# Performance work log

Hardware: AMD Instinct MI355X
Metric: run time of the kernel (lower is better)

## Reference

```python
import jax, jax.numpy as jnp
import numpy as np

B, N, D_MODEL, ATT_DIM, H = 2, 2048, 1024, 1024, 8
HEAD_DIM = ATT_DIM // H


def setup_inputs() -> dict:
    key = jax.random.key(0)
    ks = jax.random.split(key, 10)
    s_in = 1.0 / np.sqrt(D_MODEL)
    s_att = 1.0 / np.sqrt(ATT_DIM)
    x = jax.random.normal(ks[0], (B, N, D_MODEL), dtype=jnp.float32)
    mask = jax.random.randint(ks[1], (B, 1, N, N), 0, 2) == 1
    Wq = jax.random.uniform(ks[2], (D_MODEL, ATT_DIM), jnp.float32, -s_in, s_in)
    bq = jnp.zeros((ATT_DIM,), jnp.float32)
    Wk = jax.random.uniform(ks[3], (D_MODEL, ATT_DIM), jnp.float32, -s_in, s_in)
    bk = jnp.zeros((ATT_DIM,), jnp.float32)
    Wv = jax.random.uniform(ks[4], (D_MODEL, ATT_DIM), jnp.float32, -s_in, s_in)
    bv = jnp.zeros((ATT_DIM,), jnp.float32)
    Wo = jax.random.uniform(ks[5], (ATT_DIM, D_MODEL), jnp.float32, -s_att, s_att)
    bo = jnp.zeros((D_MODEL,), jnp.float32)
    return {"x": x, "mask": mask, "Wq": Wq, "bq": bq, "Wk": Wk, "bk": bk,
            "Wv": Wv, "bv": bv, "Wo": Wo, "bo": bo}


def reference(x, mask, Wq, bq, Wk, bk, Wv, bv, Wo, bo):
    # x: [B, N, d_model]; dropout is identity (eval mode) for a deterministic baseline.
    b, n, d_model = x.shape
    scale = d_model ** (-0.5)  # NOTE: original scales by d_model, not head_dim

    def split_heads(t):  # [B, N, att] -> [B, H, N, head]
        return t.reshape(b, n, H, HEAD_DIM).transpose(0, 2, 1, 3)

    q = split_heads(x @ Wq + bq)
    k = split_heads(x @ Wk + bk)
    v = split_heads(x @ Wv + bv)
    score = jnp.einsum('bhqd,bhkd->bhqk', q, k) * scale
    score = jnp.where(mask, -jnp.inf, score)
    w = jax.nn.softmax(score, axis=-1)
    out = jnp.einsum('bhqk,bhkd->bhqd', w, v)            # [B, H, N, head]
    out = out.transpose(0, 2, 1, 3).reshape(b, n, ATT_DIM)
    return out @ Wo + bo
```

## Files before the change

### kernel.cpp

```cpp
#include <hip/hip_runtime.h>
#include <stdint.h>

typedef __bf16 bf16_t;
typedef bf16_t bf16x8 __attribute__((ext_vector_type(8)));
typedef bf16_t bf16x4 __attribute__((ext_vector_type(4)));
typedef float f32x4 __attribute__((ext_vector_type(4)));
typedef unsigned long long u64;

#define B_ 2
#define N_ 2048
#define DM 1024
#define H_ 8
#define HD 128

#define GLDS16(g, l) __builtin_amdgcn_global_load_lds(                      \
    (const __attribute__((address_space(1))) void*)(g),                     \
    (__attribute__((address_space(3))) void*)(l), 16, 0, 0)

#if __has_builtin(__builtin_amdgcn_exp2f)
#define EXP2F(x) __builtin_amdgcn_exp2f(x)
#else
#define EXP2F(x) exp2f(x)
#endif

__global__ void cvt_kernel(const float* __restrict__ in, bf16_t* __restrict__ out, int n8)
{
    int i = blockIdx.x * blockDim.x + threadIdx.x;
    if (i >= n8) return;
    const float4 a = *(const float4*)(in + (size_t)i * 8);
    const float4 b = *(const float4*)(in + (size_t)i * 8 + 4);
    bf16x8 o;
    o[0] = (bf16_t)a.x; o[1] = (bf16_t)a.y; o[2] = (bf16_t)a.z; o[3] = (bf16_t)a.w;
    o[4] = (bf16_t)b.x; o[5] = (bf16_t)b.y; o[6] = (bf16_t)b.z; o[7] = (bf16_t)b.w;
    *(bf16x8*)(out + (size_t)i * 8) = o;
}

__global__ void transpose_cvt(const float* __restrict__ W, bf16_t* __restrict__ Wt)
{
    __shared__ float t[32][33];
    const int tx = threadIdx.x & 31;
    const int ty = threadIdx.x >> 5;
    const int bx = blockIdx.x * 32;
    const int by = blockIdx.y * 32;
#pragma unroll
    for (int i = 0; i < 32; i += 8)
        t[ty + i][tx] = W[(size_t)(by + ty + i) * 1024 + bx + tx];
    __syncthreads();
#pragma unroll
    for (int i = 0; i < 32; i += 8)
        Wt[(size_t)(bx + ty + i) * 1024 + by + tx] = (bf16_t)t[tx][ty + i];
}

__global__ void mask_pack(const int* __restrict__ mask, u64* __restrict__ mb, int nwords)
{
    const int t = blockIdx.x * blockDim.x + threadIdx.x;
    const int w = t >> 6;
    if (w >= nwords) return;
    const int v = mask[(size_t)w * 64 + (t & 63)];
    const u64 bits = __ballot(v != 0);
    if ((t & 63) == 0) mb[w] = bits;
}

template<int MODE>
__global__ __launch_bounds__(256)
void gemm_bt(const bf16_t* __restrict__ A, const bf16_t* __restrict__ Bt,
             const float* __restrict__ b0, const float* __restrict__ b1,
             const float* __restrict__ b2,
             void* __restrict__ Cout, bf16_t* __restrict__ VtOut,
             const int M, const int N, const int K, const int ldc, const int gy)
{
    __shared__ bf16_t sA[2][128 * 32];
    __shared__ bf16_t sB[2][128 * 32];

    const int tid  = threadIdx.x;
    const int wv   = tid >> 6;
    const int lane = tid & 63;
    const int fr   = lane & 15;
    const int fk   = (lane >> 4) * 8;

    const int nwg = gridDim.x;
    const int swz = ((int)blockIdx.x & 7) * (nwg >> 3) + ((int)blockIdx.x >> 3);
    const int by  = swz % gy;
    const int bx  = swz / gy;

    const int row0 = bx * 128;
    const int col0 = by * 128;
    const int wr   = (wv >> 1) * 64;
    const int wc   = (wv & 1) * 64;

    const int srow = wv * 32 + (lane >> 2);
    const int scol = (lane & 3) * 8;

    const bf16_t* gA0 = A  + (size_t)(row0 + srow) * K + scol;
    const bf16_t* gA1 = gA0 + (size_t)16 * K;
    const bf16_t* gB0 = Bt + (size_t)(col0 + srow) * K + scol;
    const bf16_t* gB1 = gB0 + (size_t)16 * K;

    const int ldst0 = wv * 1024;
    const int ldst1 = wv * 1024 + 512;

    f32x4 acc[4][4] = {};
    const int NT = K >> 5;

    GLDS16(gA0, &sA[0][ldst0]);
    GLDS16(gA1, &sA[0][ldst1]);
    GLDS16(gB0, &sB[0][ldst0]);
    GLDS16(gB1, &sB[0][ldst1]);
    __syncthreads();

    for (int kt = 0; kt < NT; ++kt) {
        const int cur = kt & 1;
        if (kt + 1 < NT) {
            const size_t ko = (size_t)(kt + 1) * 32;
            GLDS16(gA0 + ko, &sA[cur ^ 1][ldst0]);
            GLDS16(gA1 + ko, &sA[cur ^ 1][ldst1]);
            GLDS16(gB0 + ko, &sB[cur ^ 1][ldst0]);
            GLDS16(gB1 + ko, &sB[cur ^ 1][ldst1]);
        }
        bf16x8 af[4], bfr[4];
#pragma unroll
        for (int i = 0; i < 4; ++i)
            af[i] = *(const bf16x8*)&sA[cur][(wr + i * 16 + fr) * 32 + fk];
#pragma unroll
        for (int i = 0; i < 4; ++i)
            bfr[i] = *(const bf16x8*)&sB[cur][(wc + i * 16 + fr) * 32 + fk];
#pragma unroll
        for (int i = 0; i < 4; ++i)
#pragma unroll
            for (int j = 0; j < 4; ++j)
                acc[i][j] = __builtin_amdgcn_mfma_f32_16x16x32_bf16(af[i], bfr[j], acc[i][j], 0, 0, 0);
        __syncthreads();
    }

#pragma unroll
    for (int i = 0; i < 4; ++i) {
#pragma unroll
        for (int j = 0; j < 4; ++j) {
            const int c = col0 + wc + j * 16 + fr;
            const int seg = c >> 10;
            const float bb = (seg == 0) ? b0[c] : (seg == 1 ? b1[c - 1024] : b2[c - 2048]);
#pragma unroll
            for (int r = 0; r < 4; ++r) {
                const int row = row0 + wr + i * 16 + (lane >> 4) * 4 + r;
                const float v = acc[i][j][r] + bb;
                if constexpr (MODE == 1) {
                    ((float*)Cout)[(size_t)row * ldc + c] = v;
                } else if constexpr (MODE == 0) {
                    ((bf16_t*)Cout)[(size_t)row * ldc + c] = (bf16_t)v;
                } else {
                    if (c < 2048) {
                        ((bf16_t*)Cout)[(size_t)row * ldc + c] = (bf16_t)v;
                    } else {
                        const int ch = c - 2048;
                        const int bb_ = row >> 11;
                        const int nn  = row & 2047;
                        VtOut[((size_t)(bb_ * H_ + (ch >> 7)) * HD + (ch & 127)) * N_ + nn] = (bf16_t)v;
                    }
                }
            }
        }
    }
}

__global__ __launch_bounds__(256, 2)
void flash_attn(const bf16_t* __restrict__ QK, const bf16_t* __restrict__ Vt,
                const u64* __restrict__ mbits, bf16_t* __restrict__ AO)
{
    __shared__ bf16_t sK[2][64 * 128];
    __shared__ bf16_t sVt[2][128 * 64];
    __shared__ bf16_t sP[4][16 * 64];

    const int tid  = threadIdx.x;
    const int wv   = tid >> 6;
    const int lane = tid & 63;
    const int fr   = lane & 15;
    const int g4   = lane >> 4;
    const int fk   = g4 * 8;

    const int idx = (int)blockIdx.x >> 3;
    const int bh  = ((int)blockIdx.x & 7) * 2 + (idx >> 5);
    const int q0  = (idx & 31) * 64;
    const int b   = bh >> 3;
    const int h   = bh & 7;

    const int qrow = q0 + wv * 16 + fr;
    const size_t qoff = ((size_t)(b * N_ + qrow)) * 2048 + h * HD;
    bf16x8 qf[4];
#pragma unroll
    for (int j = 0; j < 4; ++j) {
        bf16x8 t = *(const bf16x8*)&QK[qoff + j * 32 + fk];
#pragma unroll
        for (int e = 0; e < 8; ++e) qf[j][e] = (bf16_t)((float)t[e] * 0.04508422f);
    }

    const bf16_t* kg[4]; int kdo[4];
#pragma unroll
    for (int n = 0; n < 4; ++n) {
        const int row = wv * 16 + n * 4 + g4;
        kg[n] = QK + ((size_t)(b * N_ + row)) * 2048 + 1024 + h * HD
                   + ((fr * 8) ^ ((row & 15) << 3));
        kdo[n] = (wv * 16 + n * 4) * 128;
    }
    const bf16_t* vg[4]; int vdo[4];
    {
        const int l8 = lane >> 3;
        const int c8 = (lane & 7) * 8;
#pragma unroll
        for (int n = 0; n < 4; ++n) {
            const int d = wv * 32 + n * 8 + l8;
            vg[n] = Vt + ((size_t)((b * H_ + h) * HD + d)) * N_ + (c8 ^ (l8 << 3));
            vdo[n] = (wv * 32 + n * 8) * 64;
        }
    }
    const size_t mrow = (size_t)(b * N_ + q0 + wv * 16 + fr) * 32;

    f32x4 acc_o[8] = {};
    f32x4 acc_l = {};
    bf16x8 ones_f = {};
    if (fr == 0) {
#pragma unroll
        for (int e = 0; e < 8; ++e) ones_f[e] = (bf16_t)1.0f;
    }

    const int ksw = fr << 3;
    const int vsw = (fr & 7) << 3;
    const int psw = (fr & 7) << 3;

#pragma unroll
    for (int n = 0; n < 4; ++n) {
        GLDS16(kg[n], &sK[0][kdo[n]]);
        GLDS16(vg[n], &sVt[0][vdo[n]]);
    }
    u64 mb_cur = mbits[mrow];

    for (int kc = 0; kc < 32; ++kc) {
        const int cur = kc & 1;
        __syncthreads();

        u64 mb_next = 0;
        if (kc + 1 < 32) {
#pragma unroll
            for (int n = 0; n < 4; ++n) {
                GLDS16(kg[n] + (size_t)(kc + 1) * 64 * 2048, &sK[cur ^ 1][kdo[n]]);
                GLDS16(vg[n] + (kc + 1) * 64, &sVt[cur ^ 1][vdo[n]]);
            }
            mb_next = mbits[mrow + kc + 1];
        }

        f32x4 accs[4] = {};
#pragma unroll
        for (int kf = 0; kf < 4; ++kf) {
            const int krow = kf * 16 + fr;
#pragma unroll
            for (int j = 0; j < 4; ++j) {
                bf16x8 kb = *(const bf16x8*)&sK[cur][krow * 128 + ((j * 32 + fk) ^ ksw)];
                accs[kf] = __builtin_amdgcn_mfma_f32_16x16x32_bf16(kb, qf[j], accs[kf], 0, 0, 0);
            }
        }

#pragma unroll
        for (int kf = 0; kf < 4; ++kf) {
            bf16x4 w;
#pragma unroll
            for (int r = 0; r < 4; ++r) {
                const float e = EXP2F(accs[kf][r]);
                const int kv = kf * 16 + g4 * 4 + r;
                w[r] = (bf16_t)(((mb_cur >> kv) & 1ull) ? 0.0f : e);
            }
            *(bf16x4*)&sP[wv][fr * 64 + ((kf * 16 + g4 * 4) ^ psw)] = w;
        }
        mb_cur = mb_next;

#pragma unroll
        for (int ks = 0; ks < 2; ++ks) {
            bf16x8 pf = *(const bf16x8*)&sP[wv][fr * 64 + ((ks * 32 + fk) ^ psw)];
            acc_l = __builtin_amdgcn_mfma_f32_16x16x32_bf16(pf, ones_f, acc_l, 0, 0, 0);
#pragma unroll
            for (int df = 0; df < 8; ++df) {
                const int vrow = df * 16 + fr;
                bf16x8 vb = *(const bf16x8*)&sVt[cur][vrow * 64 + ((ks * 32 + fk) ^ vsw)];
                acc_o[df] = __builtin_amdgcn_mfma_f32_16x16x32_bf16(pf, vb, acc_o[df], 0, 0, 0);
            }
        }
    }

    float inv[4];
#pragma unroll
    for (int r = 0; r < 4; ++r)
        inv[r] = 1.0f / __shfl(acc_l[r], lane & 48, 64);

#pragma unroll
    for (int df = 0; df < 8; ++df) {
#pragma unroll
        for (int r = 0; r < 4; ++r) {
            const int row = q0 + wv * 16 + g4 * 4 + r;
            AO[((size_t)(b * N_ + row)) * DM + h * HD + df * 16 + fr] =
                (bf16_t)(acc_o[df][r] * inv[r]);
        }
    }
}

extern "C" void kernel_launch(void* const* d_in, const int* in_sizes, int n_in,
                              void* d_out, int out_size, void* d_ws, size_t ws_size,
                              hipStream_t stream)
{
    const float* x  = (const float*)d_in[0];
    const int* mask = (const int*)d_in[1];
    const float* Wq = (const float*)d_in[2];
    const float* bq = (const float*)d_in[3];
    const float* Wk = (const float*)d_in[4];
    const float* bk = (const float*)d_in[5];
    const float* Wv = (const float*)d_in[6];
    const float* bv = (const float*)d_in[7];
    const float* Wo = (const float*)d_in[8];
    const float* bo = (const float*)d_in[9];
    float* out = (float*)d_out;

    const size_t MT = (size_t)B_ * N_;
    bf16_t* xb    = (bf16_t*)d_ws;
    bf16_t* Wqkvt = xb + MT * DM;
    bf16_t* Wot   = Wqkvt + (size_t)3072 * DM;
    bf16_t* QKb   = Wot + (size_t)DM * DM;
    bf16_t* Vtb   = QKb + MT * 2048;
    bf16_t* AOb   = Vtb + (size_t)B_ * H_ * HD * N_;
    u64*    mbits = (u64*)(AOb + MT * DM);

    cvt_kernel<<<2048, 256, 0, stream>>>(x, xb, (int)(MT * DM / 8));

    dim3 tg(32, 32);
    transpose_cvt<<<tg, 256, 0, stream>>>(Wq, Wqkvt);
    transpose_cvt<<<tg, 256, 0, stream>>>(Wk, Wqkvt + (size_t)DM * DM);
    transpose_cvt<<<tg, 256, 0, stream>>>(Wv, Wqkvt + (size_t)2 * DM * DM);
    transpose_cvt<<<tg, 256, 0, stream>>>(Wo, Wot);

    const int nwords = B_ * N_ * (N_ / 64);
    mask_pack<<<nwords / 4, 256, 0, stream>>>(mask, mbits, nwords);

    gemm_bt<2><<<768, 256, 0, stream>>>(
        xb, Wqkvt, bq, bk, bv, QKb, Vtb, (int)MT, 3072, DM, 2048, 24);

    flash_attn<<<512, 256, 0, stream>>>(QKb, Vtb, mbits, AOb);

    gemm_bt<1><<<256, 256, 0, stream>>>(
        AOb, Wot, bo, bo, bo, out, nullptr, (int)MT, DM, DM, DM, 8);
}
```

Measured before the change: 251.7 us.

## Split attention KV range in two with 32x32 MFMA tiles and a combine pass

Attention now gives each block 128 queries and half the key range (split-KV), writing unnormalised partial outputs and row sums. A new combine kernel adds the two halves and normalises. The inner loop moves to 32x32x16 MFMAs, keeps P in registers via permlane32 swaps instead of LDS, and sums l in registers rather than with an extra MFMA. It also merges the four weight transposes into one launch and aliases the partial buffer over the x workspace. In exchange it adds an extra kernel and an extra round trip through memory for the partial outputs.

Result: no change. 248.6 us (-1.2%).

```diff
diff --git a/kernel.cpp b/kernel.cpp
--- a/kernel.cpp
+++ b/kernel.cpp
@@ -3,8 +3,9 @@
 
 typedef __bf16 bf16_t;
 typedef bf16_t bf16x8 __attribute__((ext_vector_type(8)));
-typedef bf16_t bf16x4 __attribute__((ext_vector_type(4)));
 typedef float f32x4 __attribute__((ext_vector_type(4)));
+typedef float f32x16 __attribute__((ext_vector_type(16)));
+typedef unsigned int u32;
 typedef unsigned long long u64;
 
 #define B_ 2
@@ -16,12 +17,6 @@
 #define GLDS16(g, l) __builtin_amdgcn_global_load_lds(                      \
     (const __attribute__((address_space(1))) void*)(g),                     \
     (__attribute__((address_space(3))) void*)(l), 16, 0, 0)
-
-#if __has_builtin(__builtin_amdgcn_exp2f)
-#define EXP2F(x) __builtin_amdgcn_exp2f(x)
-#else
-#define EXP2F(x) exp2f(x)
-#endif
 
 __global__ void cvt_kernel(const float* __restrict__ in, bf16_t* __restrict__ out, int n8)
 {
@@ -35,9 +30,14 @@
     *(bf16x8*)(out + (size_t)i * 8) = o;
 }
 
-__global__ void transpose_cvt(const float* __restrict__ W, bf16_t* __restrict__ Wt)
+__global__ void transpose_cvt4(const float* __restrict__ Wq, const float* __restrict__ Wk,
+                               const float* __restrict__ Wv, const float* __restrict__ Wo,
+                               bf16_t* __restrict__ Wqkvt, bf16_t* __restrict__ Wot)
 {
     __shared__ float t[32][33];
+    const int z = blockIdx.z;
+    const float* W = (z == 0) ? Wq : (z == 1) ? Wk : (z == 2) ? Wv : Wo;
+    bf16_t* Wt = (z < 3) ? (Wqkvt + (size_t)z * DM * DM) : Wot;
     const int tx = threadIdx.x & 31;
     const int ty = threadIdx.x >> 5;
     const int bx = blockIdx.x * 32;
@@ -162,42 +162,53 @@
     }
 }
 
+__device__ __forceinline__ u32 pk2(float lo, float hi)
+{
+    union { bf16_t h[2]; u32 u; } t;
+    t.h[0] = (bf16_t)lo; t.h[1] = (bf16_t)hi;
+    return t.u;
+}
+
 __global__ __launch_bounds__(256, 2)
 void flash_attn(const bf16_t* __restrict__ QK, const bf16_t* __restrict__ Vt,
-                const u64* __restrict__ mbits, bf16_t* __restrict__ AO)
+                const u64* __restrict__ mbits, bf16_t* __restrict__ On,
+                float* __restrict__ Ls)
 {
     __shared__ bf16_t sK[2][64 * 128];
     __shared__ bf16_t sVt[2][128 * 64];
-    __shared__ bf16_t sP[4][16 * 64];
 
     const int tid  = threadIdx.x;
     const int wv   = tid >> 6;
     const int lane = tid & 63;
+    const int lq   = lane & 31;
+    const int hi   = lane >> 5;
+    const int g4   = lane >> 4;
     const int fr   = lane & 15;
-    const int g4   = lane >> 4;
-    const int fk   = g4 * 8;
-
-    const int idx = (int)blockIdx.x >> 3;
-    const int bh  = ((int)blockIdx.x & 7) * 2 + (idx >> 5);
-    const int q0  = (idx & 31) * 64;
+
+    const int wid = ((int)blockIdx.x & 7) * 64 + ((int)blockIdx.x >> 3);
+    const int s   = wid >> 8;
+    const int bh  = (wid >> 4) & 15;
+    const int qb  = wid & 15;
     const int b   = bh >> 3;
     const int h   = bh & 7;
-
-    const int qrow = q0 + wv * 16 + fr;
-    const size_t qoff = ((size_t)(b * N_ + qrow)) * 2048 + h * HD;
-    bf16x8 qf[4];
-#pragma unroll
-    for (int j = 0; j < 4; ++j) {
-        bf16x8 t = *(const bf16x8*)&QK[qoff + j * 32 + fk];
-#pragma unroll
-        for (int e = 0; e < 8; ++e) qf[j][e] = (bf16_t)((float)t[e] * 0.04508422f);
+    const int q0  = qb * 128;
+    const int kvbase = s * 1024;
+
+    const int q = q0 + wv * 32 + lq;
+    const size_t qoff = ((size_t)(b * N_ + q)) * 2048 + h * HD + hi * 8;
+    bf16x8 qf[8];
+#pragma unroll
+    for (int kk = 0; kk < 8; ++kk) {
+        bf16x8 t = *(const bf16x8*)&QK[qoff + kk * 16];
+#pragma unroll
+        for (int e = 0; e < 8; ++e) qf[kk][e] = (bf16_t)((float)t[e] * 0.04508422f);
     }
 
     const bf16_t* kg[4]; int kdo[4];
 #pragma unroll
     for (int n = 0; n < 4; ++n) {
         const int row = wv * 16 + n * 4 + g4;
-        kg[n] = QK + ((size_t)(b * N_ + row)) * 2048 + 1024 + h * HD
+        kg[n] = QK + ((size_t)(b * N_ + kvbase + row)) * 2048 + 1024 + h * HD
                    + ((fr * 8) ^ ((row & 15) << 3));
         kdo[n] = (wv * 16 + n * 4) * 128;
     }
@@ -208,96 +219,118 @@
 #pragma unroll
         for (int n = 0; n < 4; ++n) {
             const int d = wv * 32 + n * 8 + l8;
-            vg[n] = Vt + ((size_t)((b * H_ + h) * HD + d)) * N_ + (c8 ^ (l8 << 3));
+            vg[n] = Vt + ((size_t)((b * H_ + h) * HD + d)) * N_ + kvbase + (c8 ^ (l8 << 3));
             vdo[n] = (wv * 32 + n * 8) * 64;
         }
     }
-    const size_t mrow = (size_t)(b * N_ + q0 + wv * 16 + fr) * 32;
-
-    f32x4 acc_o[8] = {};
-    f32x4 acc_l = {};
-    bf16x8 ones_f = {};
-    if (fr == 0) {
-#pragma unroll
-        for (int e = 0; e < 8; ++e) ones_f[e] = (bf16_t)1.0f;
-    }
-
-    const int ksw = fr << 3;
-    const int vsw = (fr & 7) << 3;
-    const int psw = (fr & 7) << 3;
+    const size_t mrow = ((size_t)(b * N_ + q)) * 32 + s * 16;
+
+    f32x16 acc_o[4] = {};
+    float lsum = 0.0f;
+
+    const int ksw = (lq & 15) << 3;
+    const int vsw = (lq & 7) << 3;
 
 #pragma unroll
     for (int n = 0; n < 4; ++n) {
         GLDS16(kg[n], &sK[0][kdo[n]]);
         GLDS16(vg[n], &sVt[0][vdo[n]]);
     }
-    u64 mb_cur = mbits[mrow];
-
-    for (int kc = 0; kc < 32; ++kc) {
+
+    for (int kc = 0; kc < 16; ++kc) {
         const int cur = kc & 1;
         __syncthreads();
 
-        u64 mb_next = 0;
-        if (kc + 1 < 32) {
+        if (kc + 1 < 16) {
 #pragma unroll
             for (int n = 0; n < 4; ++n) {
                 GLDS16(kg[n] + (size_t)(kc + 1) * 64 * 2048, &sK[cur ^ 1][kdo[n]]);
                 GLDS16(vg[n] + (kc + 1) * 64, &sVt[cur ^ 1][vdo[n]]);
             }
-            mb_next = mbits[mrow + kc + 1];
-        }
-
-        f32x4 accs[4] = {};
-#pragma unroll
-        for (int kf = 0; kf < 4; ++kf) {
-            const int krow = kf * 16 + fr;
-#pragma unroll
-            for (int j = 0; j < 4; ++j) {
-                bf16x8 kb = *(const bf16x8*)&sK[cur][krow * 128 + ((j * 32 + fk) ^ ksw)];
-                accs[kf] = __builtin_amdgcn_mfma_f32_16x16x32_bf16(kb, qf[j], accs[kf], 0, 0, 0);
+        }
+        const u64 mb = mbits[mrow + kc];
+
+        f32x16 st0 = {}, st1 = {};
+#pragma unroll
+        for (int kk = 0; kk < 8; ++kk) {
+            const int co = (kk * 16 + hi * 8) ^ ksw;
+            bf16x8 kb0 = *(const bf16x8*)&sK[cur][lq * 128 + co];
+            bf16x8 kb1 = *(const bf16x8*)&sK[cur][(32 + lq) * 128 + co];
+            st0 = __builtin_amdgcn_mfma_f32_32x32x16_bf16(kb0, qf[kk], st0, 0, 0, 0);
+            st1 = __builtin_amdgcn_mfma_f32_32x32x16_bf16(kb1, qf[kk], st1, 0, 0, 0);
+        }
+
+        bf16x8 paf[4];
+#pragma unroll
+        for (int t32 = 0; t32 < 2; ++t32) {
+            float p[16];
+#pragma unroll
+            for (int r = 0; r < 16; ++r) {
+                const int kv = t32 * 32 + (r & 3) + 8 * (r >> 2) + 4 * hi;
+                const float e = exp2f(t32 ? st1[r] : st0[r]);
+                p[r] = ((mb >> kv) & 1ull) ? 0.0f : e;
+                lsum += p[r];
             }
-        }
-
-#pragma unroll
-        for (int kf = 0; kf < 4; ++kf) {
-            bf16x4 w;
-#pragma unroll
-            for (int r = 0; r < 4; ++r) {
-                const float e = EXP2F(accs[kf][r]);
-                const int kv = kf * 16 + g4 * 4 + r;
-                w[r] = (bf16_t)(((mb_cur >> kv) & 1ull) ? 0.0f : e);
+            u32 w0 = pk2(p[0], p[1]),   w1 = pk2(p[2], p[3]);
+            u32 w2 = pk2(p[4], p[5]),   w3 = pk2(p[6], p[7]);
+            u32 w4 = pk2(p[8], p[9]),   w5 = pk2(p[10], p[11]);
+            u32 w6 = pk2(p[12], p[13]), w7 = pk2(p[14], p[15]);
+            asm volatile("v_permlane32_swap_b32 %0, %1" : "+v"(w0), "+v"(w2));
+            asm volatile("v_permlane32_swap_b32 %0, %1" : "+v"(w1), "+v"(w3));
+            asm volatile("v_permlane32_swap_b32 %0, %1" : "+v"(w4), "+v"(w6));
+            asm volatile("v_permlane32_swap_b32 %0, %1" : "+v"(w5), "+v"(w7));
+            union { u32 u[4]; bf16x8 v; } f0, f1;
+            f0.u[0] = w0; f0.u[1] = w1; f0.u[2] = w2; f0.u[3] = w3;
+            f1.u[0] = w4; f1.u[1] = w5; f1.u[2] = w6; f1.u[3] = w7;
+            paf[t32 * 2]     = f0.v;
+            paf[t32 * 2 + 1] = f1.v;
+        }
+
+#pragma unroll
+        for (int dt = 0; dt < 4; ++dt) {
+            const int vr = (dt * 32 + lq) * 64;
+#pragma unroll
+            for (int ks = 0; ks < 4; ++ks) {
+                bf16x8 vb = *(const bf16x8*)&sVt[cur][vr + ((ks * 16 + hi * 8) ^ vsw)];
+                acc_o[dt] = __builtin_amdgcn_mfma_f32_32x32x16_bf16(paf[ks], vb, acc_o[dt], 0, 0, 0);
             }
-            *(bf16x4*)&sP[wv][fr * 64 + ((kf * 16 + g4 * 4) ^ psw)] = w;
-        }
-        mb_cur = mb_next;
-
-#pragma unroll
-        for (int ks = 0; ks < 2; ++ks) {
-            bf16x8 pf = *(const bf16x8*)&sP[wv][fr * 64 + ((ks * 32 + fk) ^ psw)];
-            acc_l = __builtin_amdgcn_mfma_f32_16x16x32_bf16(pf, ones_f, acc_l, 0, 0, 0);
-#pragma unroll
-            for (int df = 0; df < 8; ++df) {
-                const int vrow = df * 16 + fr;
-                bf16x8 vb = *(const bf16x8*)&sVt[cur][vrow * 64 + ((ks * 32 + fk) ^ vsw)];
-                acc_o[df] = __builtin_amdgcn_mfma_f32_16x16x32_bf16(pf, vb, acc_o[df], 0, 0, 0);
-            }
-        }
-    }
-
-    float inv[4];
-#pragma unroll
-    for (int r = 0; r < 4; ++r)
-        inv[r] = 1.0f / __shfl(acc_l[r], lane & 48, 64);
-
-#pragma unroll
-    for (int df = 0; df < 8; ++df) {
-#pragma unroll
-        for (int r = 0; r < 4; ++r) {
-            const int row = q0 + wv * 16 + g4 * 4 + r;
-            AO[((size_t)(b * N_ + row)) * DM + h * HD + df * 16 + fr] =
-                (bf16_t)(acc_o[df][r] * inv[r]);
-        }
-    }
+        }
+    }
+
+    lsum += __shfl_xor(lsum, 32, 64);
+
+#pragma unroll
+    for (int dt = 0; dt < 4; ++dt) {
+#pragma unroll
+        for (int r = 0; r < 16; ++r) {
+            const int qg = q0 + wv * 32 + (r & 3) + 8 * (r >> 2) + 4 * hi;
+            On[((size_t)(s * 4096 + b * N_ + qg)) * 1024 + h * HD + dt * 32 + lq] =
+                (bf16_t)acc_o[dt][r];
+        }
+    }
+    if (lane < 32)
+        Ls[((size_t)((s * 2 + b) * 8 + h)) * 2048 + q0 + wv * 32 + lane] = lsum;
+}
+
+__global__ void combine(const bf16_t* __restrict__ On, const float* __restrict__ Ls,
+                        bf16_t* __restrict__ AO)
+{
+    const int idx = blockIdx.x * 256 + threadIdx.x;
+    const int row = idx >> 7;
+    const int c8  = (idx & 127) * 8;
+    const int b = row >> 11;
+    const int n = row & 2047;
+    const int h = c8 >> 7;
+    const float l0 = Ls[((size_t)(b * 8 + h)) * 2048 + n];
+    const float l1 = Ls[((size_t)((2 + b) * 8 + h)) * 2048 + n];
+    const float w  = 1.0f / (l0 + l1);
+    bf16x8 a = *(const bf16x8*)&On[(size_t)row * 1024 + c8];
+    bf16x8 d = *(const bf16x8*)&On[(size_t)4096 * 1024 + (size_t)row * 1024 + c8];
+    bf16x8 o;
+#pragma unroll
+    for (int e = 0; e < 8; ++e)
+        o[e] = (bf16_t)(((float)a[e] + (float)d[e]) * w);
+    *(bf16x8*)&AO[(size_t)row * 1024 + c8] = o;
 }
 
 extern "C" void kernel_launch(void* const* d_in, const int* in_sizes, int n_in,
@@ -317,21 +350,21 @@
     float* out = (float*)d_out;
 
     const size_t MT = (size_t)B_ * N_;
-    bf16_t* xb    = (bf16_t*)d_ws;
-    bf16_t* Wqkvt = xb + MT * DM;
-    bf16_t* Wot   = Wqkvt + (size_t)3072 * DM;
-    bf16_t* QKb   = Wot + (size_t)DM * DM;
+    const size_t M1 = 1024 * 1024;
+    bf16_t* wsb   = (bf16_t*)d_ws;
+    bf16_t* On    = wsb;
+    bf16_t* xb    = wsb;
+    bf16_t* Wqkvt = wsb + 4 * M1;
+    bf16_t* Wot   = wsb + 8 * M1;
+    bf16_t* QKb   = wsb + 9 * M1;
     bf16_t* Vtb   = QKb + MT * 2048;
     bf16_t* AOb   = Vtb + (size_t)B_ * H_ * HD * N_;
     u64*    mbits = (u64*)(AOb + MT * DM);
+    float*  Ls    = (float*)(mbits + (size_t)B_ * N_ * 32);
 
     cvt_kernel<<<2048, 256, 0, stream>>>(x, xb, (int)(MT * DM / 8));
 
-    dim3 tg(32, 32);
-    transpose_cvt<<<tg, 256, 0, stream>>>(Wq, Wqkvt);
-    transpose_cvt<<<tg, 256, 0, stream>>>(Wk, Wqkvt + (size_t)DM * DM);
-    transpose_cvt<<<tg, 256, 0, stream>>>(Wv, Wqkvt + (size_t)2 * DM * DM);
-    transpose_cvt<<<tg, 256, 0, stream>>>(Wo, Wot);
+    transpose_cvt4<<<dim3(32, 32, 4), 256, 0, stream>>>(Wq, Wk, Wv, Wo, Wqkvt, Wot);
 
     const int nwords = B_ * N_ * (N_ / 64);
     mask_pack<<<nwords / 4, 256, 0, stream>>>(mask, mbits, nwords);
@@ -339,7 +372,9 @@
     gemm_bt<2><<<768, 256, 0, stream>>>(
         xb, Wqkvt, bq, bk, bv, QKb, Vtb, (int)MT, 3072, DM, 2048, 24);
 
-    flash_attn<<<512, 256, 0, stream>>>(QKb, Vtb, mbits, AOb);
+    flash_attn<<<512, 256, 0, stream>>>(QKb, Vtb, mbits, On, Ls);
+
+    combine<<<2048, 256, 0, stream>>>(On, Ls, AOb);
 
     gemm_bt<1><<<256, 256, 0, stream>>>(
         AOb, Wot, bo, bo, bo, out, nullptr, (int)MT, DM, DM, DM, 8);
```
